# Kernel tuning notes

Measured on AMD Instinct MI355X. Metric: run time of the kernel, lower is better.

The kernel has to match this reference:

```python
import jax, jax.numpy as jnp
import numpy as np

N, E = 100000, 800000
IN, OUT, H = 128, 128, 4
C = OUT // H            # per-head channels = 32
TP = OUT // 4           # type_proj out = 32


def _p(key, shape, fan_in):
    return jax.random.normal(key, shape, dtype=jnp.float32) / np.sqrt(fan_in)


def setup_inputs() -> dict:
    key = jax.random.key(0)
    ks = jax.random.split(key, 24)
    inp = {
        "x": jax.random.normal(ks[0], (N, IN), dtype=jnp.float32),
        "edge_index": jax.random.randint(ks[1], (2, E), 0, N, dtype=jnp.int64),
        "node_types": jax.random.normal(ks[2], (N, 2), dtype=jnp.float32),
    }
    # two GATv2 layers: lin_l, lin_r (bias=True), attention vector att, output bias
    for i, base in ((1, 3), (2, 9)):
        inp[f"Wl{i}"] = _p(ks[base + 0], (H * C, IN), IN)
        inp[f"bl{i}"] = jnp.zeros((H * C,), jnp.float32)
        inp[f"Wr{i}"] = _p(ks[base + 1], (H * C, IN), IN)
        inp[f"br{i}"] = jnp.zeros((H * C,), jnp.float32)
        inp[f"att{i}"] = _p(ks[base + 2], (H, C), C)
        inp[f"bias{i}"] = jnp.zeros((H * C,), jnp.float32)
    inp["Wt"] = _p(ks[20], (TP, 2), 2)
    inp["bt"] = jnp.zeros((TP,), jnp.float32)
    inp["Wc"] = _p(ks[21], (OUT, OUT + TP), OUT + TP)
    inp["bc"] = jnp.zeros((OUT,), jnp.float32)
    return inp


def segment_softmax(scores, seg, num_segments):
    # numerically stable softmax over edges grouped by destination node
    m = jax.ops.segment_max(scores, seg, num_segments=num_segments)
    m = jnp.where(jnp.isfinite(m), m, 0.0)  # empty segments
    ex = jnp.exp(scores - m[seg])
    s = jax.ops.segment_sum(ex, seg, num_segments=num_segments)
    return ex / (s[seg] + 1e-16)


def gatv2(x, src, dst, Wl, bl, Wr, br, att, bias):
    xl = (x @ Wl.T + bl).reshape(N, H, C)   # source transform
    xr = (x @ Wr.T + br).reshape(N, H, C)   # target transform
    m = xl[src] + xr[dst]                   # [E,H,C] per-edge message
    e = jnp.einsum('ehc,hc->eh', jax.nn.leaky_relu(m, 0.2), att)  # [E,H]
    alpha = segment_softmax(e, dst, N)
    out = jax.ops.segment_sum(alpha[..., None] * xl[src], dst, num_segments=N)
    return out.reshape(N, H * C) + bias


def reference(x, edge_index, node_types,
              Wl1, bl1, Wr1, br1, att1, bias1,
              Wl2, bl2, Wr2, br2, att2, bias2,
              Wt, bt, Wc, bc):
    src, dst = edge_index[0], edge_index[1]
    h1 = gatv2(x, src, dst, Wl1, bl1, Wr1, br1, att1, bias1)
    h2 = gatv2(x, src, dst, Wl2, bl2, Wr2, br2, att2, bias2)
    type_emb = node_types @ Wt.T + bt
    h = jnp.concatenate([h1 + h2, type_emb], axis=-1)
    return h @ Wc.T + bc
```

## Files before the change

kernel.cpp:

```cpp
#include <hip/hip_runtime.h>
#include <math.h>

#define NN 100000
#define EE 800000
static constexpr size_t N128 = (size_t)NN * 128;

__device__ __forceinline__ float lrelu(float x) { return x >= 0.f ? x : 0.2f * x; }

__global__ void k_init(int* __restrict__ deg) {
    int i = blockIdx.x * blockDim.x + threadIdx.x;
    if (i < NN) deg[i] = 0;
}

__global__ void k_hist(const int* __restrict__ ei, int* __restrict__ deg) {
    int e = blockIdx.x * blockDim.x + threadIdx.x;
    if (e < EE) {
        int dst = ei[EE + e];
        atomicAdd(&deg[dst], 1);
    }
}

__global__ void k_scanA(const int* __restrict__ deg, int* __restrict__ bsum) {
    int b = blockIdx.x, t = threadIdx.x;
    int i = b * 256 + t;
    int v = (i < NN) ? deg[i] : 0;
    #pragma unroll
    for (int d = 1; d < 64; d <<= 1) v += __shfl_xor(v, d);
    __shared__ int ws[4];
    int lane = t & 63, w = t >> 6;
    if (lane == 0) ws[w] = v;
    __syncthreads();
    if (t == 0) bsum[b] = ws[0] + ws[1] + ws[2] + ws[3];
}

__global__ void k_scanB(int* __restrict__ bsum, int* __restrict__ rowptr, int nb) {
    int lane = threadIdx.x;
    int carry = 0;
    for (int base = 0; base < nb; base += 64) {
        int i = base + lane;
        int v = (i < nb) ? bsum[i] : 0;
        int incl = v;
        #pragma unroll
        for (int d = 1; d < 64; d <<= 1) {
            int u = __shfl_up(incl, d);
            if (lane >= d) incl += u;
        }
        if (i < nb) bsum[i] = carry + incl - v;
        carry += __shfl(incl, 63);
    }
    if (lane == 0) rowptr[NN] = carry;
}

__global__ void k_scanC(int* __restrict__ deg_and_cur, int* __restrict__ rowptr,
                        const int* __restrict__ bsum) {
    int b = blockIdx.x, t = threadIdx.x;
    int i = b * 256 + t;
    int lane = t & 63, w = t >> 6;
    int v = (i < NN) ? deg_and_cur[i] : 0;
    int incl = v;
    #pragma unroll
    for (int d = 1; d < 64; d <<= 1) {
        int u = __shfl_up(incl, d);
        if (lane >= d) incl += u;
    }
    __shared__ int wtot[4];
    if (lane == 63) wtot[w] = incl;
    __syncthreads();
    int woff = 0;
    for (int k = 0; k < w; k++) woff += wtot[k];
    int excl = woff + incl - v + bsum[b];
    if (i < NN) {
        rowptr[i] = excl;
        deg_and_cur[i] = excl;
    }
}

__global__ void k_scat(const int* __restrict__ ei, int* __restrict__ cur,
                       int* __restrict__ esrc) {
    int e = blockIdx.x * blockDim.x + threadIdx.x;
    if (e < EE) {
        int src = ei[e];
        int dst = ei[EE + e];
        int pos = atomicAdd(&cur[dst], 1);
        esrc[pos] = src;
    }
}

__global__ __launch_bounds__(256) void k_gemm2(
    const float* __restrict__ x,
    const float* __restrict__ W0, const float* __restrict__ B0,
    const float* __restrict__ W1, const float* __restrict__ B1,
    float* __restrict__ o0, float* __restrict__ o1) {
    __shared__ float4 wsmT[2][8][129];
    int tid = threadIdx.x;
    int row0 = blockIdx.x * 64;
    int ty = tid >> 4, tx = tid & 15;

    int grow[4], gclamp[4];
    #pragma unroll
    for (int i = 0; i < 4; i++) {
        grow[i] = row0 + ty + 16 * i;
        gclamp[i] = grow[i] < NN ? grow[i] : NN - 1;
    }
    const float4* x4 = (const float4*)x;
    const float4* Wm4[2] = {(const float4*)W0, (const float4*)W1};

    float acc0[4][8], acc1[4][8];
    #pragma unroll
    for (int i = 0; i < 4; i++)
        #pragma unroll
        for (int j = 0; j < 8; j++) { acc0[i][j] = 0.f; acc1[i][j] = 0.f; }

    for (int kc = 0; kc < 4; kc++) {
        __syncthreads();
        #pragma unroll
        for (int q = 0; q < 8; q++) {
            int mm = q >> 2;
            int rem = (q & 3) * 256 + tid;
            int r = rem >> 3, c4 = rem & 7;
            wsmT[mm][c4][r] = Wm4[mm][r * 32 + kc * 8 + c4];
        }
        __syncthreads();
        #pragma unroll
        for (int kk = 0; kk < 8; kk++) {
            float4 a[4];
            #pragma unroll
            for (int i = 0; i < 4; i++)
                a[i] = x4[(size_t)gclamp[i] * 32 + kc * 8 + kk];
            {
                float4 b[8];
                #pragma unroll
                for (int j = 0; j < 8; j++) b[j] = wsmT[0][kk][tx + 16 * j];
                #pragma unroll
                for (int i = 0; i < 4; i++)
                    #pragma unroll
                    for (int j = 0; j < 8; j++) {
                        acc0[i][j] += a[i].x * b[j].x;
                        acc0[i][j] += a[i].y * b[j].y;
                        acc0[i][j] += a[i].z * b[j].z;
                        acc0[i][j] += a[i].w * b[j].w;
                    }
            }
            {
                float4 b[8];
                #pragma unroll
                for (int j = 0; j < 8; j++) b[j] = wsmT[1][kk][tx + 16 * j];
                #pragma unroll
                for (int i = 0; i < 4; i++)
                    #pragma unroll
                    for (int j = 0; j < 8; j++) {
                        acc1[i][j] += a[i].x * b[j].x;
                        acc1[i][j] += a[i].y * b[j].y;
                        acc1[i][j] += a[i].z * b[j].z;
                        acc1[i][j] += a[i].w * b[j].w;
                    }
            }
        }
    }
    #pragma unroll
    for (int i = 0; i < 4; i++) {
        if (grow[i] < NN) {
            #pragma unroll
            for (int j = 0; j < 8; j++) {
                int c = tx + 16 * j;
                o0[(size_t)grow[i] * 128 + c] = acc0[i][j] + B0[c];
                o1[(size_t)grow[i] * 128 + c] = acc1[i][j] + B1[c];
            }
        }
    }
}

template <int ACC>
__global__ __launch_bounds__(256) void k_edge1(
    const float* __restrict__ xl, const float* __restrict__ xr,
    const int* __restrict__ rowptr, const int* __restrict__ esrc,
    const float* __restrict__ att, const float* __restrict__ bias,
    float* __restrict__ g) {
    int wid = (blockIdx.x * blockDim.x + threadIdx.x) >> 6;
    if (wid >= NN) return;
    int lane = threadIdx.x & 63;
    int c0 = 2 * lane;
    int h = lane >> 4;
    int ch = c0 & 31;

    float2 xrv = *(const float2*)(xr + (size_t)wid * 128 + c0);
    float2 a = *(const float2*)(att + h * 32 + ch);

    int beg = rowptr[wid], end = rowptr[wid + 1];
    float s = 0.f, acc0 = 0.f, acc1 = 0.f;

    int e = beg;
    for (; e + 3 < end; e += 4) {
        int s0 = esrc[e], s1 = esrc[e + 1], s2 = esrc[e + 2], s3 = esrc[e + 3];
        float2 va = *(const float2*)(xl + (size_t)s0 * 128 + c0);
        float2 vb = *(const float2*)(xl + (size_t)s1 * 128 + c0);
        float2 vc = *(const float2*)(xl + (size_t)s2 * 128 + c0);
        float2 vd = *(const float2*)(xl + (size_t)s3 * 128 + c0);
        float ta = lrelu(va.x + xrv.x) * a.x + lrelu(va.y + xrv.y) * a.y;
        float tb = lrelu(vb.x + xrv.x) * a.x + lrelu(vb.y + xrv.y) * a.y;
        float tc = lrelu(vc.x + xrv.x) * a.x + lrelu(vc.y + xrv.y) * a.y;
        float td = lrelu(vd.x + xrv.x) * a.x + lrelu(vd.y + xrv.y) * a.y;
        #pragma unroll
        for (int d = 1; d < 16; d <<= 1) {
            ta += __shfl_xor(ta, d);
            tb += __shfl_xor(tb, d);
            tc += __shfl_xor(tc, d);
            td += __shfl_xor(td, d);
        }
        float ea = __expf(ta), eb = __expf(tb), ec = __expf(tc), ed = __expf(td);
        s += (ea + eb) + (ec + ed);
        acc0 += ea * va.x + eb * vb.x + ec * vc.x + ed * vd.x;
        acc1 += ea * va.y + eb * vb.y + ec * vc.y + ed * vd.y;
    }
    for (; e < end; ++e) {
        int s0 = esrc[e];
        float2 va = *(const float2*)(xl + (size_t)s0 * 128 + c0);
        float t = lrelu(va.x + xrv.x) * a.x + lrelu(va.y + xrv.y) * a.y;
        #pragma unroll
        for (int d = 1; d < 16; d <<= 1) t += __shfl_xor(t, d);
        float ex = __expf(t);
        s += ex;
        acc0 += ex * va.x;
        acc1 += ex * va.y;
    }
    float r = s > 0.f ? 1.f / (s + 1e-16f) : 0.f;
    float2 gv;
    gv.x = acc0 * r + bias[c0];
    gv.y = acc1 * r + bias[c0 + 1];
    float2* gp = (float2*)(g + (size_t)wid * 128 + c0);
    if (ACC) {
        float2 old = *gp;
        gv.x += old.x;
        gv.y += old.y;
    }
    *gp = gv;
}

__global__ __launch_bounds__(256) void k_final(
    const float* __restrict__ g128, const float* __restrict__ nt,
    const float* __restrict__ Wt, const float* __restrict__ bt,
    const float* __restrict__ Wc, const float* __restrict__ bc,
    float* __restrict__ out) {
    __shared__ float4 gs[64][41];
    __shared__ float4 wc[128][9];
    int tid = threadIdx.x;
    int row0 = blockIdx.x * 64;
    #pragma unroll
    for (int q = 0; q < 8; q++) {
        int idx = q * 256 + tid;
        int r = idx >> 5, c4 = idx & 31;
        int gr = row0 + r;
        float4 v = {0.f, 0.f, 0.f, 0.f};
        if (gr < NN) v = ((const float4*)g128)[(size_t)gr * 32 + c4];
        gs[r][c4] = v;
    }
    #pragma unroll
    for (int q = 0; q < 2; q++) {
        int idx = q * 256 + tid;
        int r = idx >> 3, c4 = idx & 7;
        int gr = row0 + r;
        float4 v = {0.f, 0.f, 0.f, 0.f};
        if (gr < NN) {
            float n0 = nt[2 * gr], n1 = nt[2 * gr + 1];
            #pragma unroll
            for (int u = 0; u < 4; u++) {
                int c = c4 * 4 + u;
                ((float*)&v)[u] = n0 * Wt[2 * c] + n1 * Wt[2 * c + 1] + bt[c];
            }
        }
        gs[r][32 + c4] = v;
    }
    int ty = tid >> 4, tx = tid & 15;
    float acc[4][8];
    #pragma unroll
    for (int i = 0; i < 4; i++)
        #pragma unroll
        for (int j = 0; j < 8; j++) acc[i][j] = 0.f;

    for (int kc = 0; kc < 5; kc++) {
        __syncthreads();
        #pragma unroll
        for (int q = 0; q < 4; q++) {
            int idx = q * 256 + tid;
            int r = idx >> 3, c4 = idx & 7;
            wc[r][c4] = ((const float4*)Wc)[r * 40 + kc * 8 + c4];
        }
        __syncthreads();
        #pragma unroll
        for (int kk = 0; kk < 8; kk++) {
            float4 a[4], b[8];
            #pragma unroll
            for (int i = 0; i < 4; i++) a[i] = gs[ty + 16 * i][kc * 8 + kk];
            #pragma unroll
            for (int j = 0; j < 8; j++) b[j] = wc[tx + 16 * j][kk];
            #pragma unroll
            for (int i = 0; i < 4; i++)
                #pragma unroll
                for (int j = 0; j < 8; j++) {
                    acc[i][j] += a[i].x * b[j].x;
                    acc[i][j] += a[i].y * b[j].y;
                    acc[i][j] += a[i].z * b[j].z;
                    acc[i][j] += a[i].w * b[j].w;
                }
        }
    }
    #pragma unroll
    for (int i = 0; i < 4; i++) {
        int gr = row0 + ty + 16 * i;
        if (gr < NN) {
            #pragma unroll
            for (int j = 0; j < 8; j++) {
                int c = tx + 16 * j;
                out[(size_t)gr * 128 + c] = acc[i][j] + bc[c];
            }
        }
    }
}

extern "C" void kernel_launch(void* const* d_in, const int* in_sizes, int n_in,
                              void* d_out, int out_size, void* d_ws, size_t ws_size,
                              hipStream_t stream) {
    const float* x = (const float*)d_in[0];
    const int* ei = (const int*)d_in[1];
    const float* nt = (const float*)d_in[2];
    const float* Wl1 = (const float*)d_in[3];
    const float* bl1 = (const float*)d_in[4];
    const float* Wr1 = (const float*)d_in[5];
    const float* br1 = (const float*)d_in[6];
    const float* att1 = (const float*)d_in[7];
    const float* bias1 = (const float*)d_in[8];
    const float* Wl2 = (const float*)d_in[9];
    const float* bl2 = (const float*)d_in[10];
    const float* Wr2 = (const float*)d_in[11];
    const float* br2 = (const float*)d_in[12];
    const float* att2 = (const float*)d_in[13];
    const float* bias2 = (const float*)d_in[14];
    const float* Wt = (const float*)d_in[15];
    const float* bt = (const float*)d_in[16];
    const float* Wc = (const float*)d_in[17];
    const float* bc = (const float*)d_in[18];
    float* out = (float*)d_out;

    float* ws_f = (float*)d_ws;
    float* xl = ws_f;
    float* xr = ws_f + N128;
    int* rowptr = (int*)(ws_f + 2 * N128);
    int* cur = rowptr + NN + 1;
    int* esrc = cur + NN;
    int* bsum = esrc + EE;

    const int nbN = (NN + 255) / 256;
    const int nbE = (EE + 255) / 256;
    const int nbG = (NN + 63) / 64;
    const int nbW = (NN + 3) / 4;

    k_init<<<nbN, 256, 0, stream>>>(cur);
    k_hist<<<nbE, 256, 0, stream>>>(ei, cur);
    k_scanA<<<nbN, 256, 0, stream>>>(cur, bsum);
    k_scanB<<<1, 64, 0, stream>>>(bsum, rowptr, nbN);
    k_scanC<<<nbN, 256, 0, stream>>>(cur, rowptr, bsum);
    k_scat<<<nbE, 256, 0, stream>>>(ei, cur, esrc);

    k_gemm2<<<nbG, 256, 0, stream>>>(x, Wl1, bl1, Wr1, br1, xl, xr);
    k_edge1<0><<<nbW, 256, 0, stream>>>(xl, xr, rowptr, esrc, att1, bias1, out);
    k_gemm2<<<nbG, 256, 0, stream>>>(x, Wl2, bl2, Wr2, br2, xl, xr);
    k_edge1<1><<<nbW, 256, 0, stream>>>(xl, xr, rowptr, esrc, att2, bias2, out);

    k_final<<<nbG, 256, 0, stream>>>(out, nt, Wt, bt, Wc, bc, out);
}
```

Baseline: 714.6 us.

## Use fp16 MFMA matrix cores for the GATv2 input projections

Casts x and the four projection weight matrices to fp16 in workspace, then computes both xl/xr projections per layer with 16x16x32 f16 MFMA instructions instead of the fp32 shared-memory GEMM. The goal is to cut the dense projection cost and halve the bytes read for x. The change adds two cast kernels and extra workspace, and falls back to the old path when the workspace is too small. Rounding inputs to fp16 costs some precision.

```diff
diff --git a/kernel.cpp b/kernel.cpp
--- a/kernel.cpp
+++ b/kernel.cpp
@@ -1,9 +1,14 @@
 #include <hip/hip_runtime.h>
 #include <math.h>
+#include <stdint.h>
 
 #define NN 100000
 #define EE 800000
 static constexpr size_t N128 = (size_t)NN * 128;
+
+typedef _Float16 f16x8 __attribute__((ext_vector_type(8)));
+typedef _Float16 f16x4 __attribute__((ext_vector_type(4)));
+typedef float f32x4 __attribute__((ext_vector_type(4)));
 
 __device__ __forceinline__ float lrelu(float x) { return x >= 0.f ? x : 0.2f * x; }
 
@@ -83,6 +88,70 @@
         int dst = ei[EE + e];
         int pos = atomicAdd(&cur[dst], 1);
         esrc[pos] = src;
+    }
+}
+
+__global__ void k_castx(const float* __restrict__ x, _Float16* __restrict__ xh) {
+    int i = blockIdx.x * 256 + threadIdx.x;
+    float4 v = ((const float4*)x)[i];
+    f16x4 h = {(_Float16)v.x, (_Float16)v.y, (_Float16)v.z, (_Float16)v.w};
+    *(f16x4*)(xh + 4 * (size_t)i) = h;
+}
+
+__global__ void k_castw(const float* __restrict__ W0, const float* __restrict__ W1,
+                        const float* __restrict__ W2, const float* __restrict__ W3,
+                        _Float16* __restrict__ wh) {
+    int i = blockIdx.x * 256 + threadIdx.x;
+    wh[i] = (_Float16)W0[i];
+    wh[16384 + i] = (_Float16)W1[i];
+    wh[32768 + i] = (_Float16)W2[i];
+    wh[49152 + i] = (_Float16)W3[i];
+}
+
+__global__ __launch_bounds__(256) void k_gemm_mfma(
+    const _Float16* __restrict__ xh,
+    const _Float16* __restrict__ w0, const float* __restrict__ B0,
+    const _Float16* __restrict__ w1, const float* __restrict__ B1,
+    float* __restrict__ o0, float* __restrict__ o1) {
+    int tid = threadIdx.x;
+    int wave = tid >> 6, lane = tid & 63;
+    int row0 = blockIdx.x * 64 + wave * 16;
+    int mrow = row0 + (lane & 15);
+    int mclamp = mrow < NN ? mrow : NN - 1;
+    int kb8 = (lane >> 4) * 8;
+
+    f32x4 acc[2][8];
+    #pragma unroll
+    for (int m = 0; m < 2; m++)
+        #pragma unroll
+        for (int t = 0; t < 8; t++) acc[m][t] = {0.f, 0.f, 0.f, 0.f};
+
+    #pragma unroll
+    for (int kb = 0; kb < 4; kb++) {
+        f16x8 a = *(const f16x8*)(xh + (size_t)mclamp * 128 + kb * 32 + kb8);
+        #pragma unroll
+        for (int t = 0; t < 8; t++) {
+            int wrow = t * 16 + (lane & 15);
+            f16x8 b0 = *(const f16x8*)(w0 + wrow * 128 + kb * 32 + kb8);
+            acc[0][t] = __builtin_amdgcn_mfma_f32_16x16x32_f16(a, b0, acc[0][t], 0, 0, 0);
+            f16x8 b1 = *(const f16x8*)(w1 + wrow * 128 + kb * 32 + kb8);
+            acc[1][t] = __builtin_amdgcn_mfma_f32_16x16x32_f16(a, b1, acc[1][t], 0, 0, 0);
+        }
+    }
+    int ccol = lane & 15;
+    int rbase = row0 + (lane >> 4) * 4;
+    #pragma unroll
+    for (int t = 0; t < 8; t++) {
+        int c = t * 16 + ccol;
+        float b0v = B0[c], b1v = B1[c];
+        #pragma unroll
+        for (int j = 0; j < 4; j++) {
+            int r = rbase + j;
+            if (r < NN) {
+                o0[(size_t)r * 128 + c] = acc[0][t][j] + b0v;
+                o1[(size_t)r * 128 + c] = acc[1][t][j] + b1v;
+            }
+        }
     }
 }
 
@@ -341,13 +410,17 @@
     const float* bc = (const float*)d_in[18];
     float* out = (float*)d_out;
 
-    float* ws_f = (float*)d_ws;
-    float* xl = ws_f;
-    float* xr = ws_f + N128;
-    int* rowptr = (int*)(ws_f + 2 * N128);
+    char* base = (char*)d_ws;
+    float* xl = (float*)base;
+    float* xr = xl + N128;
+    int* rowptr = (int*)(xr + N128);
     int* cur = rowptr + NN + 1;
     int* esrc = cur + NN;
     int* bsum = esrc + EE;
+    _Float16* xh = (_Float16*)(((uintptr_t)(bsum + 400) + 15) & ~(uintptr_t)15);
+    _Float16* wh = xh + N128;
+    size_t need = (size_t)((char*)(wh + 4 * 16384) - base);
+    const bool use_mfma = ws_size >= need;
 
     const int nbN = (NN + 255) / 256;
     const int nbE = (EE + 255) / 256;
@@ -361,10 +434,19 @@
     k_scanC<<<nbN, 256, 0, stream>>>(cur, rowptr, bsum);
     k_scat<<<nbE, 256, 0, stream>>>(ei, cur, esrc);
 
-    k_gemm2<<<nbG, 256, 0, stream>>>(x, Wl1, bl1, Wr1, br1, xl, xr);
-    k_edge1<0><<<nbW, 256, 0, stream>>>(xl, xr, rowptr, esrc, att1, bias1, out);
-    k_gemm2<<<nbG, 256, 0, stream>>>(x, Wl2, bl2, Wr2, br2, xl, xr);
-    k_edge1<1><<<nbW, 256, 0, stream>>>(xl, xr, rowptr, esrc, att2, bias2, out);
+    if (use_mfma) {
+        k_castx<<<12500, 256, 0, stream>>>(x, xh);
+        k_castw<<<64, 256, 0, stream>>>(Wl1, Wr1, Wl2, Wr2, wh);
+        k_gemm_mfma<<<nbG, 256, 0, stream>>>(xh, wh, bl1, wh + 16384, br1, xl, xr);
+        k_edge1<0><<<nbW, 256, 0, stream>>>(xl, xr, rowptr, esrc, att1, bias1, out);
+        k_gemm_mfma<<<nbG, 256, 0, stream>>>(xh, wh + 32768, bl2, wh + 49152, br2, xl, xr);
+        k_edge1<1><<<nbW, 256, 0, stream>>>(xl, xr, rowptr, esrc, att2, bias2, out);
+    } else {
+        k_gemm2<<<nbG, 256, 0, stream>>>(x, Wl1, bl1, Wr1, br1, xl, xr);
+        k_edge1<0><<<nbW, 256, 0, stream>>>(xl, xr, rowptr, esrc, att1, bias1, out);
+        k_gemm2<<<nbG, 256, 0, stream>>>(x, Wl2, bl2, Wr2, br2, xl, xr);
+        k_edge1<1><<<nbW, 256, 0, stream>>>(xl, xr, rowptr, esrc, att2, bias2, out);
+    }
 
     k_final<<<nbG, 256, 0, stream>>>(out, nt, Wt, bt, Wc, bc, out);
 }
```

Result: faster. 622.9 us (-12.8%).
